# Kernel optimization log

Measured on AMD Instinct MI355X. Metric: run time of the kernel, lower is better.

Reference implementation:

```python
import jax, jax.numpy as jnp
import numpy as np

B, T, D, H = 8, 2048, 1024, 128  # batch, seq (== block_size), n_embd, head_size


def setup_inputs() -> dict:
    key = jax.random.key(0)
    kx, kq, kk, kv = jax.random.split(key, 4)
    s = D ** -0.5  # rough linear-init scale
    return {
        "x": jax.random.normal(kx, (B, T, D), dtype=jnp.float32),
        "Wq": jax.random.normal(kq, (D, H), dtype=jnp.float32) * s,
        "Wk": jax.random.normal(kk, (D, H), dtype=jnp.float32) * s,
        "Wv": jax.random.normal(kv, (D, H), dtype=jnp.float32) * s,
    }


def reference(x, Wq, Wk, Wv):
    # Linear projections (no bias)
    q = x @ Wq  # [B, T, H]
    k = x @ Wk  # [B, T, H]
    v = x @ Wv  # [B, T, H]
    scale = k.shape[-1] ** -0.5
    scores = jnp.einsum("bth,bsh->bts", q, k) * scale  # [B, T, T]
    # causal mask from tril buffer
    causal = jnp.tril(jnp.ones((T, T), dtype=bool))
    scores = jnp.where(causal, scores, jnp.finfo(scores.dtype).min)
    att = jax.nn.softmax(scores, axis=-1)
    out = jnp.einsum("bts,bsh->bth", att, v)  # [B, T, H]
    return out
```

## Files before the change

### kernel.cpp

```cpp
#include <hip/hip_runtime.h>
#include <hip/hip_bf16.h>
#include <stdint.h>

typedef float f32x4 __attribute__((ext_vector_type(4)));
typedef __bf16 bf16x8 __attribute__((ext_vector_type(8)));

#define T_SEQ 2048
#define D_EMB 1024
#define H_DIM 128
#define NBATCH 8
#define NTOK 16384

typedef __attribute__((address_space(3))) uint32_t lds_u32;
typedef const __attribute__((address_space(1))) uint32_t glb_u32;

#define DPPF(x, ctrl)                                                    \
  __int_as_float(__builtin_amdgcn_update_dpp(                            \
      0, __float_as_int(x), (ctrl), 0xF, 0xF, true))

#define PIPE_FENCE()                                       \
  do {                                                     \
    asm volatile("s_waitcnt vmcnt(0)" ::: "memory");       \
    __builtin_amdgcn_s_barrier();                          \
    __builtin_amdgcn_sched_barrier(0);                     \
  } while (0)


__global__ __launch_bounds__(256) void prep_w_kernel(
    const float* __restrict__ Wq, const float* __restrict__ Wk,
    const float* __restrict__ Wv, __hip_bfloat16* __restrict__ Wt) {
  const int mat = blockIdx.x >> 7;
  const int h = blockIdx.x & 127;
  const float* W = (mat == 0) ? Wq : ((mat == 1) ? Wk : Wv);
  __hip_bfloat16* dst = Wt + (size_t)(mat * 128 + h) * D_EMB;
  for (int k = threadIdx.x; k < D_EMB; k += 256)
    dst[k] = __float2bfloat16(W[(size_t)k * H_DIM + h]);
}

__global__ __launch_bounds__(256) void proj_kernel(
    const float* __restrict__ x, const __hip_bfloat16* __restrict__ Wt,
    __hip_bfloat16* __restrict__ qb, __hip_bfloat16* __restrict__ kb,
    __hip_bfloat16* __restrict__ vt) {
  __shared__ __align__(16) float Af[2][64 * 64];
  __shared__ __align__(16) __hip_bfloat16 Bs[2][192 * 64];
  const int tid = threadIdx.x;
  const int wave = tid >> 6;
  const int lane = tid & 63;
  const int g = lane >> 4;
  const int lr = lane & 15;
  const int hh = blockIdx.x & 1;
  const int m0 = (blockIdx.x >> 1) * 64;
  const int wcl = wave * 48;
  const __hip_bfloat16* WtH = Wt + (size_t)hh * 192 * D_EMB;

  f32x4 acc[4][3];
#pragma unroll
  for (int m = 0; m < 4; ++m)
#pragma unroll
    for (int n = 0; n < 3; ++n) acc[m][n] = f32x4{0.f, 0.f, 0.f, 0.f};

  auto stageA = [&](int buf, int k0) {
#pragma unroll
    for (int i = 0; i < 4; ++i) {
      const int e = i * 256 + tid;
      const int row = e >> 4;
      const int un = e & 15;
      __builtin_amdgcn_global_load_lds(
          (glb_u32*)(uintptr_t)(x + (size_t)(m0 + row) * D_EMB + k0 +
                                ((un ^ (row & 15)) * 4)),
          (lds_u32*)(uintptr_t)(&Af[buf][e * 4]), 16, 0, 0);
    }
  };
  auto stageB = [&](int buf, int k0) {
#pragma unroll
    for (int i = 0; i < 6; ++i) {
      const int u = i * 256 + tid;
      const int row = u >> 3;
      const int chunk = u & 7;
      __builtin_amdgcn_global_load_lds(
          (glb_u32*)(uintptr_t)(WtH + (size_t)row * D_EMB + k0 +
                                ((chunk ^ (row & 7)) * 8)),
          (lds_u32*)(uintptr_t)(&Bs[buf][row * 64 + chunk * 8]), 16, 0, 0);
    }
  };
  auto compute = [&](int buf) {
#pragma unroll
    for (int kk = 0; kk < 2; ++kk) {
      bf16x8 a[4];
#pragma unroll
      for (int m = 0; m < 4; ++m) {
        const int row = m * 16 + lr;
        const int u0 = kk * 8 + g * 2;
        const f32x4 lo = *reinterpret_cast<const f32x4*>(
            &Af[buf][row * 64 + ((u0 ^ (row & 15)) * 4)]);
        const f32x4 hi = *reinterpret_cast<const f32x4*>(
            &Af[buf][row * 64 + (((u0 + 1) ^ (row & 15)) * 4)]);
        union { bf16x8 v; __hip_bfloat16 h[8]; } u;
        u.h[0] = __float2bfloat16(lo[0]);
        u.h[1] = __float2bfloat16(lo[1]);
        u.h[2] = __float2bfloat16(lo[2]);
        u.h[3] = __float2bfloat16(lo[3]);
        u.h[4] = __float2bfloat16(hi[0]);
        u.h[5] = __float2bfloat16(hi[1]);
        u.h[6] = __float2bfloat16(hi[2]);
        u.h[7] = __float2bfloat16(hi[3]);
        a[m] = u.v;
      }
#pragma unroll
      for (int n = 0; n < 3; ++n) {
        const int row = wcl + n * 16 + lr;
        bf16x8 b = *reinterpret_cast<const bf16x8*>(
            &Bs[buf][row * 64 + (((kk * 4 + g) ^ (row & 7)) * 8)]);
#pragma unroll
        for (int m = 0; m < 4; ++m)
          acc[m][n] =
              __builtin_amdgcn_mfma_f32_16x16x32_bf16(a[m], b, acc[m][n], 0, 0, 0);
      }
    }
  };

  stageA(0, 0);
  stageB(0, 0);

  int cur = 0;
  for (int k = 0; k < 16; ++k) {
    PIPE_FENCE();
    if (k < 15) {
      stageA(cur ^ 1, (k + 1) * 64);
      stageB(cur ^ 1, (k + 1) * 64);
    }
    compute(cur);
    cur ^= 1;
  }

#pragma unroll
  for (int n = 0; n < 3; ++n) {
    const int ng = hh * 192 + wcl + n * 16 + lr;
    const int head = ng >> 7;
    const int h = ng & 127;
#pragma unroll
    for (int m = 0; m < 4; ++m) {
#pragma unroll
      for (int r = 0; r < 4; ++r) {
        const int row = m0 + m * 16 + g * 4 + r;
        const __hip_bfloat16 val = __float2bfloat16(acc[m][n][r]);
        if (head == 0) {
          qb[(size_t)row * H_DIM + h] = val;
        } else if (head == 1) {
          kb[(size_t)row * H_DIM + h] = val;
        } else {
          const int bi = row >> 11;
          const int t = row & (T_SEQ - 1);
          vt[((size_t)bi * H_DIM + h) * T_SEQ + t] = val;
        }
      }
    }
  }
}

__global__ __launch_bounds__(512) void attn_kernel(
    const __hip_bfloat16* __restrict__ qb, const __hip_bfloat16* __restrict__ kb,
    const __hip_bfloat16* __restrict__ vt, float* __restrict__ out,
    float* __restrict__ PA_O, float* __restrict__ PA_ml,
    float* __restrict__ PB_O, float* __restrict__ PB_ml) {
  __shared__ __align__(16) __hip_bfloat16 KV[2][16384];
  __shared__ __align__(16) __hip_bfloat16 Pl[8][16][40];
  __shared__ float Obuf[4][16][132];
  __shared__ float mbuf[8][16];
  __shared__ float lbuf[8][16];

  const int tid = threadIdx.x;
  const int wave = tid >> 6;
  const int lane = tid & 63;
  const int g = lane >> 4;
  const int lr = lane & 15;
  const int qt = wave >> 1;
  const int kp = wave & 1;
  const int idx = blockIdx.x;
  const int b = idx & 7;
  const int u = idx >> 3;

  const __hip_bfloat16* qB = qb + (size_t)b * T_SEQ * H_DIM;
  const __hip_bfloat16* kB = kb + (size_t)b * T_SEQ * H_DIM;
  const __hip_bfloat16* vB = vt + (size_t)b * H_DIM * T_SEQ;
  const float scale = 0.08838834764831845f;

  auto stage = [&](__hip_bfloat16* buf, int s0) {
#pragma unroll
    for (int i = 0; i < 2; ++i) {
      const int uu = tid + i * 512;
      const int row = uu >> 4, grp = uu & 15;
      __builtin_amdgcn_global_load_lds(
          (glb_u32*)(uintptr_t)(kB + (size_t)(s0 + row) * H_DIM +
                                ((grp ^ (row & 15)) * 8)),
          (lds_u32*)(uintptr_t)(buf + uu * 8), 16, 0, 0);
    }
#pragma unroll
    for (int i = 0; i < 2; ++i) {
      const int uu = tid + i * 512;
      const int h = uu >> 3, grp = uu & 7;
      __builtin_amdgcn_global_load_lds(
          (glb_u32*)(uintptr_t)(vB + (size_t)h * T_SEQ + s0 +
                                ((grp ^ (h & 7)) * 8)),
          (lds_u32*)(uintptr_t)(buf + 8192 + uu * 8), 16, 0, 0);
    }
  };

  auto process = [&](int tile, int rr0, int rr1, int mode) {
    const int qrow0 = tile * 64 + qt * 16;
    bf16x8 qf[4];
#pragma unroll
    for (int kt = 0; kt < 4; ++kt)
      qf[kt] = *reinterpret_cast<const bf16x8*>(
          qB + (size_t)(qrow0 + lr) * H_DIM + kt * 32 + g * 8);

    f32x4 oacc[8];
#pragma unroll
    for (int i = 0; i < 8; ++i) oacc[i] = f32x4{0.f, 0.f, 0.f, 0.f};
    float mrow[4] = {-1e30f, -1e30f, -1e30f, -1e30f};
    float lrow[4] = {0.f, 0.f, 0.f, 0.f};

    __hip_bfloat16* bufA = &KV[0][0];
    __hip_bfloat16* bufB = &KV[1][0];
    stage(bufA, rr0 * 64);

    for (int r = rr0; r <= rr1; ++r) {
      PIPE_FENCE();
      if (r < rr1) stage(bufB, (r + 1) * 64);
      const int s0 = r * 64;
      const bool active = (s0 + kp * 32) <= (qrow0 + 15);
      if (active) {
        f32x4 sacc[2];
        sacc[0] = f32x4{0.f, 0.f, 0.f, 0.f};
        sacc[1] = f32x4{0.f, 0.f, 0.f, 0.f};
#pragma unroll
        for (int nt = 0; nt < 2; ++nt) {
          const int kl = kp * 32 + nt * 16 + lr;
          const __hip_bfloat16* kr = bufA + kl * 128;
#pragma unroll
          for (int kt = 0; kt < 4; ++kt) {
            bf16x8 kf = *reinterpret_cast<const bf16x8*>(
                kr + (((kt * 4 + g) ^ (kl & 15)) * 8));
            sacc[nt] = __builtin_amdgcn_mfma_f32_16x16x32_bf16(qf[kt], kf,
                                                               sacc[nt], 0, 0, 0);
          }
        }
        bf16x8 vf[8];
#pragma unroll
        for (int ht = 0; ht < 8; ++ht) {
          const int h = ht * 16 + lr;
          vf[ht] = *reinterpret_cast<const bf16x8*>(
              bufA + 8192 + h * 64 + (((kp * 4 + g) ^ (h & 7)) * 8));
        }
        float sv[2][4];
#pragma unroll
        for (int nt = 0; nt < 2; ++nt)
#pragma unroll
          for (int rr = 0; rr < 4; ++rr) {
            const int key = s0 + kp * 32 + nt * 16 + lr;
            const int qr = qrow0 + g * 4 + rr;
            const float s = sacc[nt][rr] * scale;
            sv[nt][rr] = (key > qr) ? -1e30f : s;
          }
        float pm[4];
#pragma unroll
        for (int rr = 0; rr < 4; ++rr) pm[rr] = fmaxf(sv[0][rr], sv[1][rr]);
#pragma unroll
        for (int rr = 0; rr < 4; ++rr) {
          pm[rr] = fmaxf(pm[rr], DPPF(pm[rr], 0xB1));
          pm[rr] = fmaxf(pm[rr], DPPF(pm[rr], 0x4E));
          pm[rr] = fmaxf(pm[rr], DPPF(pm[rr], 0x141));
          pm[rr] = fmaxf(pm[rr], DPPF(pm[rr], 0x140));
        }
        bool ok = true;
#pragma unroll
        for (int rr = 0; rr < 4; ++rr) ok = ok && (pm[rr] <= mrow[rr] + 8.f);
        if (!__all((int)ok)) {
#pragma unroll
          for (int rr = 0; rr < 4; ++rr) {
            const float mnew = fmaxf(mrow[rr], pm[rr]);
            const float corr = __expf(mrow[rr] - mnew);
            mrow[rr] = mnew;
            lrow[rr] *= corr;
#pragma unroll
            for (int ht = 0; ht < 8; ++ht) oacc[ht][rr] *= corr;
          }
        }
        float rs[4];
#pragma unroll
        for (int rr = 0; rr < 4; ++rr) {
          const float p0 = __expf(sv[0][rr] - mrow[rr]);
          const float p1 = __expf(sv[1][rr] - mrow[rr]);
          Pl[wave][g * 4 + rr][lr] = __float2bfloat16(p0);
          Pl[wave][g * 4 + rr][16 + lr] = __float2bfloat16(p1);
          rs[rr] = p0 + p1;
        }
#pragma unroll
        for (int rr = 0; rr < 4; ++rr) {
          rs[rr] += DPPF(rs[rr], 0xB1);
          rs[rr] += DPPF(rs[rr], 0x4E);
          rs[rr] += DPPF(rs[rr], 0x141);
          rs[rr] += DPPF(rs[rr], 0x140);
        }
#pragma unroll
        for (int rr = 0; rr < 4; ++rr) lrow[rr] += rs[rr];
        bf16x8 pf = *reinterpret_cast<const bf16x8*>(&Pl[wave][lr][g * 8]);
#pragma unroll
        for (int ht = 0; ht < 8; ++ht)
          oacc[ht] = __builtin_amdgcn_mfma_f32_16x16x32_bf16(pf, vf[ht],
                                                             oacc[ht], 0, 0, 0);
      }
      __hip_bfloat16* t = bufA; bufA = bufB; bufB = t;
    }

    __syncthreads();
    if (kp == 1) {
#pragma unroll
      for (int ht = 0; ht < 8; ++ht)
#pragma unroll
        for (int rr = 0; rr < 4; ++rr)
          Obuf[qt][g * 4 + rr][ht * 16 + lr] = oacc[ht][rr];
      if (lr == 0) {
#pragma unroll
        for (int rr = 0; rr < 4; ++rr) {
          mbuf[wave][g * 4 + rr] = mrow[rr];
          lbuf[wave][g * 4 + rr] = lrow[rr];
        }
      }
    }
    __syncthreads();
    if (kp == 0) {
#pragma unroll
      for (int rr = 0; rr < 4; ++rr) {
        const float mB = mbuf[wave + 1][g * 4 + rr];
        const float lB = lbuf[wave + 1][g * 4 + rr];
        const float M = fmaxf(mrow[rr], mB);
        const float a = __expf(mrow[rr] - M);
        const float bt = __expf(mB - M);
        lrow[rr] = a * lrow[rr] + bt * lB;
        mrow[rr] = M;
#pragma unroll
        for (int ht = 0; ht < 8; ++ht)
          oacc[ht][rr] =
              a * oacc[ht][rr] + bt * Obuf[qt][g * 4 + rr][ht * 16 + lr];
      }
      if (mode == 0) {
#pragma unroll
        for (int ht = 0; ht < 8; ++ht)
#pragma unroll
          for (int rr = 0; rr < 4; ++rr) {
            const int qr = qrow0 + g * 4 + rr;
            out[((size_t)b * T_SEQ + qr) * H_DIM + ht * 16 + lr] =
                oacc[ht][rr] / lrow[rr];
          }
      } else {
        float* PO = (mode == 1) ? PA_O : PB_O;
        float* Pm = (mode == 1) ? PA_ml : PB_ml;
        const int slot = tile - 16;
#pragma unroll
        for (int rr = 0; rr < 4; ++rr) {
          const size_t pr = (size_t)(b * 16 + slot) * 64 + qt * 16 + g * 4 + rr;
#pragma unroll
          for (int ht = 0; ht < 8; ++ht)
            PO[pr * 128 + ht * 16 + lr] = oacc[ht][rr];
          if (lr == 0) {
            Pm[pr * 2 + 0] = mrow[rr];
            Pm[pr * 2 + 1] = lrow[rr];
          }
        }
      }
    }
    __syncthreads();
  };

  if (u < 16) {
    process(u, 0, u, 0);
    process(31 - u, 0, 15 - u, 1);
  } else {
    const int v = u - 16;
    process(31 - v, 16 - v, 31 - v, 2);
  }
}

__global__ __launch_bounds__(256) void combine_kernel(
    const float* __restrict__ PA_O, const float* __restrict__ PA_ml,
    const float* __restrict__ PB_O, const float* __restrict__ PB_ml,
    float* __restrict__ out) {
  const int b = blockIdx.x >> 4;
  const int s = blockIdx.x & 15;
  const int tid = threadIdx.x;
  const int row = tid >> 2;
  const int c0 = (tid & 3) * 32;
  const size_t pr = (size_t)(b * 16 + s) * 64 + row;
  const float mA = PA_ml[pr * 2], lA = PA_ml[pr * 2 + 1];
  const float mB = PB_ml[pr * 2], lB = PB_ml[pr * 2 + 1];
  const float M = fmaxf(mA, mB);
  const float a = __expf(mA - M), bb = __expf(mB - M);
  const float inv = 1.f / (a * lA + bb * lB);
  const float* oa = PA_O + pr * 128 + c0;
  const float* ob = PB_O + pr * 128 + c0;
  float* op = out + ((size_t)b * T_SEQ + (16 + s) * 64 + row) * H_DIM + c0;
#pragma unroll
  for (int i = 0; i < 32; i += 4) {
    const float4 x = *reinterpret_cast<const float4*>(oa + i);
    const float4 y = *reinterpret_cast<const float4*>(ob + i);
    float4 z;
    z.x = (a * x.x + bb * y.x) * inv;
    z.y = (a * x.y + bb * y.y) * inv;
    z.z = (a * x.z + bb * y.z) * inv;
    z.w = (a * x.w + bb * y.w) * inv;
    *reinterpret_cast<float4*>(op + i) = z;
  }
}

extern "C" void kernel_launch(void* const* d_in, const int* in_sizes, int n_in,
                              void* d_out, int out_size, void* d_ws, size_t ws_size,
                              hipStream_t stream) {
  const float* x = (const float*)d_in[0];
  const float* Wq = (const float*)d_in[1];
  const float* Wk = (const float*)d_in[2];
  const float* Wv = (const float*)d_in[3];
  float* out = (float*)d_out;

  __hip_bfloat16* Wt = (__hip_bfloat16*)d_ws;
  __hip_bfloat16* qbuf = Wt + (size_t)3 * 128 * 1024;
  __hip_bfloat16* kbuf = qbuf + (size_t)NTOK * H_DIM;
  __hip_bfloat16* vbuf = kbuf + (size_t)NTOK * H_DIM;
  float* fbase = (float*)(vbuf + (size_t)NBATCH * H_DIM * T_SEQ);
  float* PA_O = fbase;
  float* PA_ml = PA_O + (size_t)1048576;
  float* PB_O = PA_ml + 16384;
  float* PB_ml = PB_O + (size_t)1048576;

  hipLaunchKernelGGL(prep_w_kernel, dim3(384), dim3(256), 0, stream, Wq, Wk, Wv, Wt);
  hipLaunchKernelGGL(proj_kernel, dim3(512), dim3(256), 0, stream, x, Wt, qbuf,
                     kbuf, vbuf);
  hipLaunchKernelGGL(attn_kernel, dim3(256), dim3(512), 0, stream, qbuf, kbuf,
                     vbuf, out, PA_O, PA_ml, PB_O, PB_ml);
  hipLaunchKernelGGL(combine_kernel, dim3(128), dim3(256), 0, stream, PA_O,
                     PA_ml, PB_O, PB_ml, out);
}
```

Before: 75.51 us.

## Retile projection GEMM to 128x96 blocks and read x directly from global

The projection kernel drops LDS staging of the fp32 x tile. Each wave now loads its A fragments straight from global memory and converts them to bf16 in registers. The block tile becomes 128 rows by 96 output columns, laid out as a 2x2 wave grid, with a block index swizzle so the four column-quarter blocks of an M tile run close together and share x in cache. LDS use is cut to the weight buffer, which allows 3 blocks per CU under the new launch bound. The cost is that A loads are no longer asynchronous, so their latency is exposed inside compute, and x may be fetched more than once from L2.

```diff
diff --git a/kernel.cpp b/kernel.cpp
--- a/kernel.cpp
+++ b/kernel.cpp
@@ -37,21 +37,24 @@
     dst[k] = __float2bfloat16(W[(size_t)k * H_DIM + h]);
 }
 
-__global__ __launch_bounds__(256) void proj_kernel(
+__global__ __launch_bounds__(256, 3) void proj_kernel(
     const float* __restrict__ x, const __hip_bfloat16* __restrict__ Wt,
     __hip_bfloat16* __restrict__ qb, __hip_bfloat16* __restrict__ kb,
     __hip_bfloat16* __restrict__ vt) {
-  __shared__ __align__(16) float Af[2][64 * 64];
-  __shared__ __align__(16) __hip_bfloat16 Bs[2][192 * 64];
+  __shared__ __align__(16) __hip_bfloat16 Bs[2][96 * 64];
   const int tid = threadIdx.x;
   const int wave = tid >> 6;
   const int lane = tid & 63;
   const int g = lane >> 4;
   const int lr = lane & 15;
-  const int hh = blockIdx.x & 1;
-  const int m0 = (blockIdx.x >> 1) * 64;
-  const int wcl = wave * 48;
-  const __hip_bfloat16* WtH = Wt + (size_t)hh * 192 * D_EMB;
+  const int idx = blockIdx.x;
+  const int mtile = (idx & 7) | ((idx >> 5) << 3);
+  const int nq = (idx >> 3) & 3;
+  const int m0 = mtile * 128;
+  const int wr = (wave >> 1) * 64;
+  const int wcl = (wave & 1) * 48;
+  const __hip_bfloat16* WtH = Wt + (size_t)nq * 96 * D_EMB;
+  const float* xA = x + (size_t)m0 * D_EMB;
 
   f32x4 acc[4][3];
 #pragma unroll
@@ -59,21 +62,9 @@
 #pragma unroll
     for (int n = 0; n < 3; ++n) acc[m][n] = f32x4{0.f, 0.f, 0.f, 0.f};
 
-  auto stageA = [&](int buf, int k0) {
-#pragma unroll
-    for (int i = 0; i < 4; ++i) {
-      const int e = i * 256 + tid;
-      const int row = e >> 4;
-      const int un = e & 15;
-      __builtin_amdgcn_global_load_lds(
-          (glb_u32*)(uintptr_t)(x + (size_t)(m0 + row) * D_EMB + k0 +
-                                ((un ^ (row & 15)) * 4)),
-          (lds_u32*)(uintptr_t)(&Af[buf][e * 4]), 16, 0, 0);
-    }
-  };
   auto stageB = [&](int buf, int k0) {
 #pragma unroll
-    for (int i = 0; i < 6; ++i) {
+    for (int i = 0; i < 3; ++i) {
       const int u = i * 256 + tid;
       const int row = u >> 3;
       const int chunk = u & 7;
@@ -83,34 +74,33 @@
           (lds_u32*)(uintptr_t)(&Bs[buf][row * 64 + chunk * 8]), 16, 0, 0);
     }
   };
-  auto compute = [&](int buf) {
+
+  auto compute = [&](int buf, int k0) {
 #pragma unroll
     for (int kk = 0; kk < 2; ++kk) {
       bf16x8 a[4];
 #pragma unroll
       for (int m = 0; m < 4; ++m) {
-        const int row = m * 16 + lr;
-        const int u0 = kk * 8 + g * 2;
-        const f32x4 lo = *reinterpret_cast<const f32x4*>(
-            &Af[buf][row * 64 + ((u0 ^ (row & 15)) * 4)]);
-        const f32x4 hi = *reinterpret_cast<const f32x4*>(
-            &Af[buf][row * 64 + (((u0 + 1) ^ (row & 15)) * 4)]);
+        const int row = wr + m * 16 + lr;
+        const float* src = xA + (size_t)row * D_EMB + k0 + kk * 32 + g * 8;
+        const float4 lo = *reinterpret_cast<const float4*>(src);
+        const float4 hi = *reinterpret_cast<const float4*>(src + 4);
         union { bf16x8 v; __hip_bfloat16 h[8]; } u;
-        u.h[0] = __float2bfloat16(lo[0]);
-        u.h[1] = __float2bfloat16(lo[1]);
-        u.h[2] = __float2bfloat16(lo[2]);
-        u.h[3] = __float2bfloat16(lo[3]);
-        u.h[4] = __float2bfloat16(hi[0]);
-        u.h[5] = __float2bfloat16(hi[1]);
-        u.h[6] = __float2bfloat16(hi[2]);
-        u.h[7] = __float2bfloat16(hi[3]);
+        u.h[0] = __float2bfloat16(lo.x);
+        u.h[1] = __float2bfloat16(lo.y);
+        u.h[2] = __float2bfloat16(lo.z);
+        u.h[3] = __float2bfloat16(lo.w);
+        u.h[4] = __float2bfloat16(hi.x);
+        u.h[5] = __float2bfloat16(hi.y);
+        u.h[6] = __float2bfloat16(hi.z);
+        u.h[7] = __float2bfloat16(hi.w);
         a[m] = u.v;
       }
 #pragma unroll
       for (int n = 0; n < 3; ++n) {
-        const int row = wcl + n * 16 + lr;
+        const int col = wcl + n * 16 + lr;
         bf16x8 b = *reinterpret_cast<const bf16x8*>(
-            &Bs[buf][row * 64 + (((kk * 4 + g) ^ (row & 7)) * 8)]);
+            &Bs[buf][col * 64 + (((kk * 4 + g) ^ (col & 7)) * 8)]);
 #pragma unroll
         for (int m = 0; m < 4; ++m)
           acc[m][n] =
@@ -119,30 +109,28 @@
     }
   };
 
-  stageA(0, 0);
   stageB(0, 0);
 
-  int cur = 0;
-  for (int k = 0; k < 16; ++k) {
+#pragma unroll 1
+  for (int k = 0; k < 16; k += 2) {
     PIPE_FENCE();
-    if (k < 15) {
-      stageA(cur ^ 1, (k + 1) * 64);
-      stageB(cur ^ 1, (k + 1) * 64);
-    }
-    compute(cur);
-    cur ^= 1;
+    stageB(1, (k + 1) * 64);
+    compute(0, k * 64);
+    PIPE_FENCE();
+    if (k + 2 < 16) stageB(0, (k + 2) * 64);
+    compute(1, (k + 1) * 64);
   }
 
 #pragma unroll
   for (int n = 0; n < 3; ++n) {
-    const int ng = hh * 192 + wcl + n * 16 + lr;
+    const int ng = nq * 96 + wcl + n * 16 + lr;
     const int head = ng >> 7;
     const int h = ng & 127;
 #pragma unroll
     for (int m = 0; m < 4; ++m) {
 #pragma unroll
       for (int r = 0; r < 4; ++r) {
-        const int row = m0 + m * 16 + g * 4 + r;
+        const int row = m0 + wr + m * 16 + g * 4 + r;
         const __hip_bfloat16 val = __float2bfloat16(acc[m][n][r]);
         if (head == 0) {
           qb[(size_t)row * H_DIM + h] = val;
```

After: 128.9 us. 70.8% more time.

## Retile projection GEMM to 128x128 tiles and drop LDS double buffering

Applied to the files above, without the earlier changes.

The projection kernel now computes 128-row by 128-column output tiles (one of Q/K/V per block) with a 2x2 wave layout and 4x4 MFMA fragments per wave, instead of 64x192 tiles. Each staged x tile is therefore reused across fewer output columns, but each weight tile across more rows. The double-buffered async pipeline is replaced by a single buffer with two __syncthreads per k-step, which removes the overlap of loads with compute. The grid shrinks from 512 to 384 blocks, which lowers parallelism on a 256-CU device and may leave tail imbalance.

```diff
diff --git a/kernel.cpp b/kernel.cpp
--- a/kernel.cpp
+++ b/kernel.cpp
@@ -41,60 +41,62 @@
     const float* __restrict__ x, const __hip_bfloat16* __restrict__ Wt,
     __hip_bfloat16* __restrict__ qb, __hip_bfloat16* __restrict__ kb,
     __hip_bfloat16* __restrict__ vt) {
-  __shared__ __align__(16) float Af[2][64 * 64];
-  __shared__ __align__(16) __hip_bfloat16 Bs[2][192 * 64];
+  __shared__ __align__(16) float Af[128 * 64];
+  __shared__ __align__(16) __hip_bfloat16 Bs[128 * 64];
   const int tid = threadIdx.x;
   const int wave = tid >> 6;
   const int lane = tid & 63;
   const int g = lane >> 4;
   const int lr = lane & 15;
-  const int hh = blockIdx.x & 1;
-  const int m0 = (blockIdx.x >> 1) * 64;
-  const int wcl = wave * 48;
-  const __hip_bfloat16* WtH = Wt + (size_t)hh * 192 * D_EMB;
-
-  f32x4 acc[4][3];
+  const int ntile = blockIdx.x % 3;
+  const int mtile = blockIdx.x / 3;
+  const int m0 = mtile * 128;
+  const int wm = (wave >> 1) * 64;
+  const int wn = (wave & 1) * 64;
+  const __hip_bfloat16* WtT = Wt + (size_t)ntile * 128 * D_EMB;
+  const float* xA = x + (size_t)m0 * D_EMB;
+
+  f32x4 acc[4][4];
 #pragma unroll
   for (int m = 0; m < 4; ++m)
 #pragma unroll
-    for (int n = 0; n < 3; ++n) acc[m][n] = f32x4{0.f, 0.f, 0.f, 0.f};
-
-  auto stageA = [&](int buf, int k0) {
-#pragma unroll
-    for (int i = 0; i < 4; ++i) {
+    for (int n = 0; n < 4; ++n) acc[m][n] = f32x4{0.f, 0.f, 0.f, 0.f};
+
+  auto stage = [&](int k0) {
+#pragma unroll
+    for (int i = 0; i < 8; ++i) {
       const int e = i * 256 + tid;
       const int row = e >> 4;
       const int un = e & 15;
       __builtin_amdgcn_global_load_lds(
-          (glb_u32*)(uintptr_t)(x + (size_t)(m0 + row) * D_EMB + k0 +
+          (glb_u32*)(uintptr_t)(xA + (size_t)row * D_EMB + k0 +
                                 ((un ^ (row & 15)) * 4)),
-          (lds_u32*)(uintptr_t)(&Af[buf][e * 4]), 16, 0, 0);
-    }
-  };
-  auto stageB = [&](int buf, int k0) {
-#pragma unroll
-    for (int i = 0; i < 6; ++i) {
+          (lds_u32*)(uintptr_t)(&Af[e * 4]), 16, 0, 0);
+    }
+#pragma unroll
+    for (int i = 0; i < 4; ++i) {
       const int u = i * 256 + tid;
       const int row = u >> 3;
       const int chunk = u & 7;
       __builtin_amdgcn_global_load_lds(
-          (glb_u32*)(uintptr_t)(WtH + (size_t)row * D_EMB + k0 +
+          (glb_u32*)(uintptr_t)(WtT + (size_t)row * D_EMB + k0 +
                                 ((chunk ^ (row & 7)) * 8)),
-          (lds_u32*)(uintptr_t)(&Bs[buf][row * 64 + chunk * 8]), 16, 0, 0);
+          (lds_u32*)(uintptr_t)(&Bs[row * 64 + chunk * 8]), 16, 0, 0);
     }
   };
-  auto compute = [&](int buf) {
+
+  auto compute = [&]() {
 #pragma unroll
     for (int kk = 0; kk < 2; ++kk) {
       bf16x8 a[4];
 #pragma unroll
       for (int m = 0; m < 4; ++m) {
-        const int row = m * 16 + lr;
+        const int row = wm + m * 16 + lr;
         const int u0 = kk * 8 + g * 2;
         const f32x4 lo = *reinterpret_cast<const f32x4*>(
-            &Af[buf][row * 64 + ((u0 ^ (row & 15)) * 4)]);
+            &Af[row * 64 + ((u0 ^ (row & 15)) * 4)]);
         const f32x4 hi = *reinterpret_cast<const f32x4*>(
-            &Af[buf][row * 64 + (((u0 + 1) ^ (row & 15)) * 4)]);
+            &Af[row * 64 + (((u0 + 1) ^ (row & 15)) * 4)]);
         union { bf16x8 v; __hip_bfloat16 h[8]; } u;
         u.h[0] = __float2bfloat16(lo[0]);
         u.h[1] = __float2bfloat16(lo[1]);
@@ -107,10 +109,10 @@
         a[m] = u.v;
       }
 #pragma unroll
-      for (int n = 0; n < 3; ++n) {
-        const int row = wcl + n * 16 + lr;
+      for (int n = 0; n < 4; ++n) {
+        const int col = wn + n * 16 + lr;
         bf16x8 b = *reinterpret_cast<const bf16x8*>(
-            &Bs[buf][row * 64 + (((kk * 4 + g) ^ (row & 7)) * 8)]);
+            &Bs[col * 64 + (((kk * 4 + g) ^ (col & 7)) * 8)]);
 #pragma unroll
         for (int m = 0; m < 4; ++m)
           acc[m][n] =
@@ -119,30 +121,23 @@
     }
   };
 
-  stageA(0, 0);
-  stageB(0, 0);
-
-  int cur = 0;
   for (int k = 0; k < 16; ++k) {
-    PIPE_FENCE();
-    if (k < 15) {
-      stageA(cur ^ 1, (k + 1) * 64);
-      stageB(cur ^ 1, (k + 1) * 64);
-    }
-    compute(cur);
-    cur ^= 1;
+    __syncthreads();
+    stage(k * 64);
+    __syncthreads();
+    compute();
   }
 
 #pragma unroll
-  for (int n = 0; n < 3; ++n) {
-    const int ng = hh * 192 + wcl + n * 16 + lr;
+  for (int n = 0; n < 4; ++n) {
+    const int ng = ntile * 128 + wn + n * 16 + lr;
     const int head = ng >> 7;
     const int h = ng & 127;
 #pragma unroll
     for (int m = 0; m < 4; ++m) {
 #pragma unroll
       for (int r = 0; r < 4; ++r) {
-        const int row = m0 + m * 16 + g * 4 + r;
+        const int row = m0 + wm + m * 16 + g * 4 + r;
         const __hip_bfloat16 val = __float2bfloat16(acc[m][n][r]);
         if (head == 0) {
           qb[(size_t)row * H_DIM + h] = val;
@@ -433,7 +428,7 @@
   float* PB_ml = PB_O + (size_t)1048576;
 
   hipLaunchKernelGGL(prep_w_kernel, dim3(384), dim3(256), 0, stream, Wq, Wk, Wv, Wt);
-  hipLaunchKernelGGL(proj_kernel, dim3(512), dim3(256), 0, stream, x, Wt, qbuf,
+  hipLaunchKernelGGL(proj_kernel, dim3(384), dim3(256), 0, stream, x, Wt, qbuf,
                      kbuf, vbuf);
   hipLaunchKernelGGL(attn_kernel, dim3(256), dim3(512), 0, stream, qbuf, kbuf,
                      vbuf, out, PA_O, PA_ml, PB_O, PB_ml);
```

New measurement: 86.67 us. 1.15x slower.
